# Kernel tuning notes

Measured on AMD Instinct MI355X. Metric: run time of the kernel, lower is better.

Reference implementation:

```python
import jax, jax.numpy as jnp
import numpy as np

VOCAB = 50000
WORD_DIM = 300
ENT_DIM = 128
ATT_DIM = 256
B, QLEN, DLEN = 64, 32, 2048
MUS = np.array([-0.9, -0.7, -0.5, -0.3, -0.1, 0.1, 0.3, 0.5, 0.7, 0.9, 1.0], dtype=np.float32)
SIGMAS = np.array([0.1] * 10 + [0.001], dtype=np.float32)


def setup_inputs() -> dict:
    key = jax.random.key(0)
    ks = jax.random.split(key, 12)
    # tokens in [-1, VOCAB-2]; -1 is padding (embed uses tok+1)
    query_tok = jax.random.randint(ks[0], (B, QLEN), -1, VOCAB - 1)
    doc_tok = jax.random.randint(ks[1], (B, DLEN), -1, VOCAB - 1)
    query_entity = jax.random.normal(ks[2], (B, QLEN, ENT_DIM), dtype=jnp.float32)
    doc_entity = jax.random.normal(ks[3], (B, DLEN, ENT_DIM), dtype=jnp.float32)
    embed_table = jax.random.normal(ks[4], (VOCAB, WORD_DIM), dtype=jnp.float32) * 0.1
    W_t = jax.random.normal(ks[5], (WORD_DIM, ATT_DIM), dtype=jnp.float32) * (1.0 / np.sqrt(WORD_DIM))
    b_t = jax.random.normal(ks[6], (ATT_DIM,), dtype=jnp.float32) * 0.01
    W_e = jax.random.normal(ks[7], (ENT_DIM, ATT_DIM), dtype=jnp.float32) * (1.0 / np.sqrt(ENT_DIM))
    b_e = jax.random.normal(ks[8], (ATT_DIM,), dtype=jnp.float32) * 0.01
    W_c = jax.random.normal(ks[9], (len(MUS), 1), dtype=jnp.float32) * 0.3
    b_c = jax.random.normal(ks[10], (1,), dtype=jnp.float32) * 0.01
    return {
        "query_tok": query_tok, "doc_tok": doc_tok,
        "query_entity": query_entity, "doc_entity": doc_entity,
        "embed_table": embed_table,
        "W_t": W_t, "b_t": b_t, "W_e": W_e, "b_e": b_e,
        "W_c": W_c, "b_c": b_c,
    }


def reference(query_tok, doc_tok, query_entity, doc_entity,
              embed_table, W_t, b_t, W_e, b_e, W_c, b_c):
    mus = jnp.asarray(MUS)
    sigmas = jnp.asarray(SIGMAS)
    # encode: embed(tok + 1)
    q_reps = embed_table[query_tok + 1]            # [B,Q,WORD]
    d_reps = embed_table[doc_tok + 1]              # [B,D,WORD]
    # transform_embed: relu(Linear(word) + Linear(entity))
    q = jax.nn.relu(q_reps @ W_t + b_t + query_entity @ W_e + b_e)  # [B,Q,A]
    d = jax.nn.relu(d_reps @ W_t + b_t + doc_entity @ W_e + b_e)    # [B,D,A]
    # SimmatModule: masked cosine similarity, VIEWS = 1
    qn = jnp.linalg.norm(q, axis=2)[:, :, None] + 1e-9              # [B,Q,1]
    dn = jnp.linalg.norm(d, axis=2)[:, None, :] + 1e-9              # [B,1,D]
    sim = jnp.einsum('bqa,bda->bqd', q, d) / (qn * dn)              # [B,Q,D]
    sim = jnp.where(query_tok[:, :, None] == -1, 0.0, sim)
    sim = jnp.where(doc_tok[:, None, :] == -1, 0.0, sim)
    # RBF kernel bank: exp(-0.5*(sim-mu)^2/sigma^2) -> [B,K,Q,D]
    adj = sim[:, None, :, :] - mus[None, :, None, None]
    kern = jnp.exp(-0.5 * adj * adj / (sigmas * sigmas)[None, :, None, None])
    result = kern.sum(axis=3)                                       # [B,K,Q]
    mask = (sim.sum(axis=2) != 0.0)[:, None, :]                     # [B,1,Q]
    mask = jnp.broadcast_to(mask, result.shape)
    result = jnp.where(mask, jnp.log(result + 1e-6), mask.astype(result.dtype))
    result = result.sum(axis=2)                                     # [B,K]
    scores = result @ W_c + b_c                                     # [B,1]
    return scores
```

## Files before the change

kernel.cpp:

```cpp
#include <hip/hip_runtime.h>
#include <math.h>

#define B_    64
#define QLEN  32
#define DLEN  2048
#define WORD  300
#define ENT   128
#define AD    256
#define NK    11
#define VOCAB 50000

typedef __bf16 bf16x8 __attribute__((ext_vector_type(8)));
typedef __bf16 bf16x4 __attribute__((ext_vector_type(4)));
typedef float  f32x4  __attribute__((ext_vector_type(4)));

__global__ __launch_bounds__(256) void knrm_wpack(
    const float* __restrict__ Wt, const float* __restrict__ We,
    const float* __restrict__ bt, const float* __restrict__ be,
    __bf16* __restrict__ Wtp, __bf16* __restrict__ Wep,
    float* __restrict__ bias)
{
    const int idx = blockIdx.x * 256 + threadIdx.x;
    if (idx < AD) bias[idx] = bt[idx] + be[idx];
    const int tile = idx >> 6, l = idx & 63;
    bf16x8 h;
    if (tile < 160) {
        const int s = tile >> 4, nb = tile & 15;
        const int col = nb * 16 + (l & 15);
        const int k0  = s * 32 + (l >> 4) * 8;
        #pragma unroll
        for (int j = 0; j < 8; ++j) {
            const int k = k0 + j;
            h[j] = (__bf16)((k < WORD) ? Wt[(size_t)k * AD + col] : 0.f);
        }
        *(bf16x8*)((char*)Wtp + (size_t)idx * 16) = h;
    } else {
        const int t2 = tile - 160;
        const int s = t2 >> 4, nb = t2 & 15;
        const int col = nb * 16 + (l & 15);
        const int k0  = s * 32 + (l >> 4) * 8;
        #pragma unroll
        for (int j = 0; j < 8; ++j)
            h[j] = (__bf16)We[(size_t)(k0 + j) * AD + col];
        *(bf16x8*)((char*)Wep + (size_t)(idx - 10240) * 16) = h;
    }
}

__global__ __launch_bounds__(256) void knrm_pgemm(
    const float* __restrict__ emb,
    const __bf16* __restrict__ Wtp,
    char* __restrict__ P)
{
    __shared__ __align__(16) char sm[40960];
    const int tid = threadIdx.x;
    const int v0  = blockIdx.x * 64;

    #pragma unroll
    for (int u = 0; u < 20; ++u) {
        const int idx  = u * 256 + tid;
        const int r    = idx / 80;
        const int slot = idx - r * 80;
        const int k    = slot * 4;
        f32x4 v = (f32x4){0.f, 0.f, 0.f, 0.f};
        if (k < WORD && v0 + r < VOCAB)
            v = *(const f32x4*)(emb + (size_t)(v0 + r) * WORD + k);
        bf16x4 hv;
        #pragma unroll
        for (int c = 0; c < 4; ++c) hv[c] = (__bf16)v[c];
        *(bf16x4*)(sm + ((r * 640 + slot * 8) ^ ((r & 7) << 4))) = hv;
    }
    __syncthreads();

    const int w  = tid >> 6;
    const int l  = tid & 63;
    const int lr = l & 15;
    const int lg = l >> 4;

    f32x4 acc[4][4];
    #pragma unroll
    for (int mf = 0; mf < 4; ++mf)
        #pragma unroll
        for (int nf = 0; nf < 4; ++nf)
            acc[mf][nf] = (f32x4){0.f, 0.f, 0.f, 0.f};

    #pragma unroll
    for (int t = 0; t < 10; ++t) {
        bf16x8 a[4];
        #pragma unroll
        for (int mf = 0; mf < 4; ++mf) {
            const int row = mf * 16 + lr;
            a[mf] = *(const bf16x8*)(sm +
                ((row * 640 + t * 64 + lg * 16) ^ ((row & 7) << 4)));
        }
        bf16x8 wv[4];
        #pragma unroll
        for (int nf = 0; nf < 4; ++nf) {
            const int tile = t * 16 + w * 4 + nf;
            wv[nf] = *(const bf16x8*)((const char*)Wtp + (size_t)tile * 1024 + l * 16);
        }
        #pragma unroll
        for (int mf = 0; mf < 4; ++mf)
            #pragma unroll
            for (int nf = 0; nf < 4; ++nf)
                acc[mf][nf] = __builtin_amdgcn_mfma_f32_16x16x32_bf16(
                    a[mf], wv[nf], acc[mf][nf], 0, 0, 0);
    }

    #pragma unroll
    for (int mf = 0; mf < 4; ++mf)
        #pragma unroll
        for (int reg = 0; reg < 4; ++reg) {
            const int v = v0 + mf * 16 + lg * 4 + reg;
            if (v < VOCAB) {
                bf16x4 h;
                #pragma unroll
                for (int nf = 0; nf < 4; ++nf) h[nf] = (__bf16)acc[mf][nf][reg];
                *(bf16x4*)(P + (size_t)v * 512 + w * 128 + lr * 8) = h;
            }
        }
}

__global__ __launch_bounds__(256) void knrm_qtrans(
    const int* __restrict__ tok,
    const float* __restrict__ ent,
    const char* __restrict__ Pp,
    const __bf16* __restrict__ Wep,
    const float* __restrict__ bias,
    char* __restrict__ qhatF)
{
    __shared__ __align__(16) char sm[16384 + 256];
    float* ssq  = (float*)(sm + 16384);
    int*   toks = (int*)(sm + 16384 + 128);

    const int tid  = threadIdx.x;
    const int row0 = blockIdx.x * 32;
    if (tid < 32) { toks[tid] = tok[row0 + tid] + 1; ssq[tid] = 0.f; }
    __syncthreads();

    const int wN = tid >> 6;
    const int l  = tid & 63;
    const int lr = l & 15;
    const int lg = l >> 4;
    const float* __restrict__ ebase = ent + (size_t)row0 * ENT;

    f32x4 acc[2][4];
    #pragma unroll
    for (int mf = 0; mf < 2; ++mf)
        #pragma unroll
        for (int nf = 0; nf < 4; ++nf)
            acc[mf][nf] = (f32x4){0.f, 0.f, 0.f, 0.f};

    bf16x4 pv[2][4];
    #pragma unroll
    for (int mf = 0; mf < 2; ++mf)
        #pragma unroll
        for (int reg = 0; reg < 4; ++reg) {
            const int r = mf * 16 + lg * 4 + reg;
            pv[mf][reg] = *(const bf16x4*)(Pp +
                (size_t)toks[r] * 512 + wN * 128 + lr * 8);
        }

    #pragma unroll
    for (int t = 0; t < 4; ++t) {
        bf16x8 a[2];
        #pragma unroll
        for (int mf = 0; mf < 2; ++mf) {
            const float* rp = ebase + (size_t)(mf * 16 + lr) * ENT + t * 32 + lg * 8;
            const f32x4 u0 = *(const f32x4*)rp;
            const f32x4 u1 = *(const f32x4*)(rp + 4);
            #pragma unroll
            for (int c = 0; c < 4; ++c) {
                a[mf][c]     = (__bf16)u0[c];
                a[mf][c + 4] = (__bf16)u1[c];
            }
        }
        bf16x8 wv[4];
        #pragma unroll
        for (int nf = 0; nf < 4; ++nf) {
            const int tile = t * 16 + wN * 4 + nf;
            wv[nf] = *(const bf16x8*)((const char*)Wep + (size_t)tile * 1024 + l * 16);
        }
        #pragma unroll
        for (int mf = 0; mf < 2; ++mf)
            #pragma unroll
            for (int nf = 0; nf < 4; ++nf)
                acc[mf][nf] = __builtin_amdgcn_mfma_f32_16x16x32_bf16(
                    a[mf], wv[nf], acc[mf][nf], 0, 0, 0);
    }

    float bv[4];
    #pragma unroll
    for (int nf = 0; nf < 4; ++nf) bv[nf] = bias[wN * 64 + nf * 16 + lr];
    float sq[2][4];
    #pragma unroll
    for (int mf = 0; mf < 2; ++mf)
        #pragma unroll
        for (int reg = 0; reg < 4; ++reg) {
            float s = 0.f;
            #pragma unroll
            for (int nf = 0; nf < 4; ++nf) {
                const float v = fmaxf(acc[mf][nf][reg] + (float)pv[mf][reg][nf]
                                      + bv[nf], 0.f);
                acc[mf][nf][reg] = v;
                s = fmaf(v, v, s);
            }
            sq[mf][reg] = s;
        }
    #pragma unroll
    for (int m = 1; m <= 8; m <<= 1)
        #pragma unroll
        for (int mf = 0; mf < 2; ++mf)
            #pragma unroll
            for (int reg = 0; reg < 4; ++reg)
                sq[mf][reg] += __shfl_xor(sq[mf][reg], m, 64);
    if (lr == 0) {
        #pragma unroll
        for (int mf = 0; mf < 2; ++mf)
            #pragma unroll
            for (int reg = 0; reg < 4; ++reg)
                atomicAdd(&ssq[mf * 16 + lg * 4 + reg], sq[mf][reg]);
    }
    #pragma unroll
    for (int mf = 0; mf < 2; ++mf)
        #pragma unroll
        for (int nf = 0; nf < 4; ++nf)
            #pragma unroll
            for (int reg = 0; reg < 4; ++reg) {
                const int r    = mf * 16 + lg * 4 + reg;
                const int col  = wN * 64 + nf * 16 + lr;
                const int byte = (r * 512 + col * 2) ^ ((r & 7) << 4);
                *(__bf16*)(sm + byte) = (__bf16)acc[mf][nf][reg];
            }
    __syncthreads();

    char* qb = qhatF + (size_t)blockIdx.x * 16384;
    #pragma unroll
    for (int it = 0; it < 4; ++it) {
        const int idx = it * 256 + tid;
        const int tile = idx >> 6, l2 = idx & 63;
        const int s  = tile >> 1, qt = tile & 1;
        const int row = qt * 16 + (l2 & 15);
        const int k0  = s * 32 + (l2 >> 4) * 8;
        const int byte = (row * 512 + k0 * 2) ^ ((row & 7) << 4);
        bf16x8 hv = *(const bf16x8*)(sm + byte);
        const float rn = (toks[row] == 0) ? 0.f
                                          : 1.f / (sqrtf(ssq[row]) + 1e-9f);
        #pragma unroll
        for (int j = 0; j < 8; ++j) hv[j] = (__bf16)((float)hv[j] * rn);
        *(bf16x8*)(qb + tile * 1024 + l2 * 16) = hv;
    }
}

__global__ __launch_bounds__(256) void knrm_fused2(
    const int* __restrict__ dtok,
    const float* __restrict__ dent,
    const char* __restrict__ Pp,
    const __bf16* __restrict__ Wep,
    const float* __restrict__ bias,
    const char* __restrict__ qhatF,
    float* __restrict__ ksum,
    float* __restrict__ simsum)
{
    __shared__ __align__(16) char sm[16384 + 256];
    float* ssq  = (float*)(sm + 16384);
    int*   toks = (int*)(sm + 16384 + 128);

    const int tid = threadIdx.x;
    const int b   = blockIdx.y;
    const int d0  = blockIdx.x * 32;
    const int drow0 = b * DLEN + d0;
    const int w  = tid >> 6;
    const int l  = tid & 63;
    const int lr = l & 15;
    const int lg = l >> 4;

    if (tid < 32) { toks[tid] = dtok[drow0 + tid] + 1; ssq[tid] = 0.f; }

    #pragma unroll
    for (int u = 0; u < 4; ++u) {
        const int slot = u * 256 + tid;
        const int r    = slot >> 5;
        const int c4   = (slot & 31) * 4;
        const f32x4 v = *(const f32x4*)(dent + (size_t)(drow0 + r) * ENT + c4);
        bf16x4 hv;
        #pragma unroll
        for (int c = 0; c < 4; ++c) hv[c] = (__bf16)v[c];
        *(bf16x4*)(sm + ((r * 256 + c4 * 2) ^ ((r & 7) << 4))) = hv;
    }
    __syncthreads();

    bf16x4 pv[2][4];
    #pragma unroll
    for (int mf = 0; mf < 2; ++mf)
        #pragma unroll
        for (int reg = 0; reg < 4; ++reg) {
            const int doc = mf * 16 + lg * 4 + reg;
            pv[mf][reg] = *(const bf16x4*)(Pp +
                (size_t)toks[doc] * 512 + w * 128 + lr * 8);
        }

    f32x4 acc[2][4];
    #pragma unroll
    for (int mf = 0; mf < 2; ++mf)
        #pragma unroll
        for (int nf = 0; nf < 4; ++nf)
            acc[mf][nf] = (f32x4){0.f, 0.f, 0.f, 0.f};

    #pragma unroll
    for (int t = 0; t < 4; ++t) {
        bf16x8 a[2];
        #pragma unroll
        for (int mf = 0; mf < 2; ++mf) {
            const int row = mf * 16 + lr;
            a[mf] = *(const bf16x8*)(sm +
                ((row * 256 + t * 64 + lg * 16) ^ ((row & 7) << 4)));
        }
        bf16x8 wv[4];
        #pragma unroll
        for (int nf = 0; nf < 4; ++nf) {
            const int tile = t * 16 + w * 4 + nf;
            wv[nf] = *(const bf16x8*)((const char*)Wep + (size_t)tile * 1024 + l * 16);
        }
        #pragma unroll
        for (int mf = 0; mf < 2; ++mf)
            #pragma unroll
            for (int nf = 0; nf < 4; ++nf)
                acc[mf][nf] = __builtin_amdgcn_mfma_f32_16x16x32_bf16(
                    a[mf], wv[nf], acc[mf][nf], 0, 0, 0);
    }
    __syncthreads();

    float bv[4];
    #pragma unroll
    for (int nf = 0; nf < 4; ++nf) bv[nf] = bias[w * 64 + nf * 16 + lr];
    float sq[2][4];
    #pragma unroll
    for (int mf = 0; mf < 2; ++mf)
        #pragma unroll
        for (int reg = 0; reg < 4; ++reg) {
            float s = 0.f;
            #pragma unroll
            for (int nf = 0; nf < 4; ++nf) {
                const float v = fmaxf(acc[mf][nf][reg] + (float)pv[mf][reg][nf]
                                      + bv[nf], 0.f);
                acc[mf][nf][reg] = v;
                s = fmaf(v, v, s);
            }
            sq[mf][reg] = s;
        }
    #pragma unroll
    for (int m = 1; m <= 8; m <<= 1)
        #pragma unroll
        for (int mf = 0; mf < 2; ++mf)
            #pragma unroll
            for (int reg = 0; reg < 4; ++reg)
                sq[mf][reg] += __shfl_xor(sq[mf][reg], m, 64);
    if (lr == 0) {
        #pragma unroll
        for (int mf = 0; mf < 2; ++mf)
            #pragma unroll
            for (int reg = 0; reg < 4; ++reg)
                atomicAdd(&ssq[mf * 16 + lg * 4 + reg], sq[mf][reg]);
    }
    #pragma unroll
    for (int mf = 0; mf < 2; ++mf)
        #pragma unroll
        for (int nf = 0; nf < 4; ++nf)
            #pragma unroll
            for (int reg = 0; reg < 4; ++reg) {
                const int doc  = mf * 16 + lg * 4 + reg;
                const int col  = w * 64 + nf * 16 + lr;
                const int byte = doc * 512 + ((col * 2) ^ ((doc & 15) << 4));
                *(__bf16*)(sm + byte) = (__bf16)acc[mf][nf][reg];
            }
    __syncthreads();

    const int dtile = w & 1, qtile = w >> 1;
    const int tdoc  = dtile * 16 + lr;
    const int q     = qtile * 16 + lr;
    const char* __restrict__ qb = qhatF + (size_t)b * 16384;
    f32x4 s0 = (f32x4){0.f, 0.f, 0.f, 0.f};
    #pragma unroll
    for (int s = 0; s < 8; ++s) {
        const bf16x8 ta = *(const bf16x8*)(sm +
            (tdoc * 512 + ((s * 64 + lg * 16) ^ ((tdoc & 15) << 4))));
        const bf16x8 qv = *(const bf16x8*)(qb + (s * 2 + qtile) * 1024 + l * 16);
        s0 = __builtin_amdgcn_mfma_f32_16x16x32_bf16(ta, qv, s0, 0, 0, 0);
    }

    float kq[12];
    #pragma unroll
    for (int k = 0; k < 12; ++k) kq[k] = 0.f;
    #pragma unroll
    for (int reg = 0; reg < 4; ++reg) {
        const int doc = dtile * 16 + lg * 4 + reg;
        const float dnv = (toks[doc] == 0) ? 0.f
                                           : 1.f / (sqrtf(ssq[doc]) + 1e-9f);
        const float sv = s0[reg] * dnv;
        kq[11] += sv;
        const float v5 = __expf(fmaf(10.f, sv, -50.f * sv * sv));
        const float gU = __expf(20.f * sv);
        const float gD = __expf(-20.f * sv);
        float u = v5;
        kq[5] += u * 0.60653066f;
        u *= gD; kq[4] += u * 0.60653066f;
        u *= gD; kq[3] += u * 0.011108997f;
        u *= gD; kq[2] += u * 3.7266532e-06f;
        u *= gD; kq[1] += u * 2.2895532e-11f;
        u *= gD; kq[0] += u * 2.5767571e-18f;
        u = v5;
        u *= gU; kq[6] += u * 0.011108997f;
        u *= gU; kq[7] += u * 3.7266532e-06f;
        u *= gU; kq[8] += u * 2.2895532e-11f;
        u *= gU; kq[9] += u * 2.5767571e-18f;
        const float t10 = sv - 1.0f;
        kq[10] += __expf(-500000.f * t10 * t10);
    }
    #pragma unroll
    for (int m = 16; m <= 32; m <<= 1)
        #pragma unroll
        for (int k = 0; k < 12; ++k)
            kq[k] += __shfl_xor(kq[k], m, 64);
    if (lg == 0) {
        #pragma unroll
        for (int k = 0; k < NK; ++k)
            atomicAdd(&ksum[((size_t)b * NK + k) * QLEN + q], kq[k]);
        atomicAdd(&simsum[b * QLEN + q], kq[11]);
    }
}

__global__ __launch_bounds__(384) void knrm_final(
    const float* __restrict__ ksum,
    const float* __restrict__ simsum,
    const float* __restrict__ Wc, const float* __restrict__ bc,
    float* __restrict__ out)
{
    __shared__ float redq[NK][QLEN];
    __shared__ float res[NK];
    const int b = blockIdx.x;
    const int t = threadIdx.x;
    if (t < NK * QLEN) {
        const int k = t >> 5;
        const int q = t & 31;
        const float ms = simsum[b * QLEN + q];
        redq[k][q] = (ms != 0.0f)
            ? logf(ksum[((size_t)b * NK + k) * QLEN + q] + 1e-6f)
            : 0.0f;
    }
    __syncthreads();
    if (t < NK) {
        float s = 0.f;
        for (int q = 0; q < QLEN; ++q) s += redq[t][q];
        res[t] = s;
    }
    __syncthreads();
    if (t == 0) {
        float s = bc[0];
        for (int k = 0; k < NK; ++k) s += res[k] * Wc[k];
        out[b] = s;
    }
}

extern "C" void kernel_launch(void* const* d_in, const int* in_sizes, int n_in,
                              void* d_out, int out_size, void* d_ws, size_t ws_size,
                              hipStream_t stream)
{
    (void)in_sizes; (void)n_in; (void)out_size; (void)ws_size;
    const int*   qtok = (const int*)d_in[0];
    const int*   dtok = (const int*)d_in[1];
    const float* qent = (const float*)d_in[2];
    const float* dent = (const float*)d_in[3];
    const float* emb  = (const float*)d_in[4];
    const float* Wt   = (const float*)d_in[5];
    const float* bt   = (const float*)d_in[6];
    const float* We   = (const float*)d_in[7];
    const float* be   = (const float*)d_in[8];
    const float* Wc   = (const float*)d_in[9];
    const float* bc   = (const float*)d_in[10];
    float* out = (float*)d_out;

    char* ws = (char*)d_ws;
    const size_t off_qhat = 0;
    const size_t off_Wtp  = off_qhat + 1048576;
    const size_t off_Wep  = off_Wtp  + 163840;
    const size_t off_bias = off_Wep  + 65536;
    const size_t off_ksum = off_bias + 1024;
    const size_t off_sim  = off_ksum + 90112;
    const size_t off_P    = off_sim  + 8192;

    char*   qhatF = ws + off_qhat;
    __bf16* Wtp   = (__bf16*)(ws + off_Wtp);
    __bf16* Wep   = (__bf16*)(ws + off_Wep);
    float*  bias  = (float*)(ws + off_bias);
    float*  ksum  = (float*)(ws + off_ksum);
    float*  simsum= (float*)(ws + off_sim);
    char*   P     = ws + off_P;

    hipMemsetAsync(ksum, 0, (size_t)(90112 + 8192), stream);

    knrm_wpack<<<dim3(56), dim3(256), 0, stream>>>(Wt, We, bt, be, Wtp, Wep, bias);
    knrm_pgemm<<<dim3((VOCAB + 63) / 64), dim3(256), 0, stream>>>(emb, Wtp, P);
    knrm_qtrans<<<dim3(64), dim3(256), 0, stream>>>(
        qtok, qent, P, Wep, bias, qhatF);
    knrm_fused2<<<dim3(DLEN / 32, B_), dim3(256), 0, stream>>>(
        dtok, dent, P, Wep, bias, qhatF, ksum, simsum);
    knrm_final<<<dim3(B_), dim3(384), 0, stream>>>(ksum, simsum, Wc, bc, out);
}
```

Baseline: 90.52 us.

## Process four doc tiles per block with register-prefetched double-buffered entity loads

The fused doc kernel now loops over four 32-doc tiles per block instead of one. While the current tile is computed, it prefetches the next tile's entity rows and projected-embedding rows into registers, then writes them into an alternate shared-memory buffer. The goal is to hide global-load latency and amortise per-block setup such as bias loads and launch overhead. In exchange the grid shrinks fourfold, to 1024 blocks, shared memory roughly doubles, and register pressure rises, all of which can hurt occupancy.

```diff
diff --git a/kernel.cpp b/kernel.cpp
--- a/kernel.cpp
+++ b/kernel.cpp
@@ -9,6 +9,7 @@
 #define AD    256
 #define NK    11
 #define VOCAB 50000
+#define TPB   4
 
 typedef __bf16 bf16x8 __attribute__((ext_vector_type(8)));
 typedef __bf16 bf16x4 __attribute__((ext_vector_type(4)));
@@ -251,7 +252,7 @@
     }
 }
 
-__global__ __launch_bounds__(256) void knrm_fused2(
+__global__ __launch_bounds__(256) void knrm_fused3(
     const int* __restrict__ dtok,
     const float* __restrict__ dent,
     const char* __restrict__ Pp,
@@ -261,20 +262,21 @@
     float* __restrict__ ksum,
     float* __restrict__ simsum)
 {
-    __shared__ __align__(16) char sm[16384 + 256];
-    float* ssq  = (float*)(sm + 16384);
-    int*   toks = (int*)(sm + 16384 + 128);
+    __shared__ __align__(16) char sm[33536];
+    float* ssqb = (float*)(sm + 32768);
+    int*   toks = (int*)(sm + 33024);
 
     const int tid = threadIdx.x;
     const int b   = blockIdx.y;
-    const int d0  = blockIdx.x * 32;
+    const int d0  = blockIdx.x * (TPB * 32);
     const int drow0 = b * DLEN + d0;
     const int w  = tid >> 6;
     const int l  = tid & 63;
     const int lr = l & 15;
     const int lg = l >> 4;
 
-    if (tid < 32) { toks[tid] = dtok[drow0 + tid] + 1; ssq[tid] = 0.f; }
+    if (tid < TPB * 32) toks[tid] = dtok[drow0 + tid] + 1;
+    if (tid < 64) ssqb[tid] = 0.f;
 
     #pragma unroll
     for (int u = 0; u < 4; ++u) {
@@ -299,133 +301,185 @@
                 (size_t)toks[doc] * 512 + w * 128 + lr * 8);
         }
 
-    f32x4 acc[2][4];
-    #pragma unroll
-    for (int mf = 0; mf < 2; ++mf)
-        #pragma unroll
-        for (int nf = 0; nf < 4; ++nf)
-            acc[mf][nf] = (f32x4){0.f, 0.f, 0.f, 0.f};
-
-    #pragma unroll
-    for (int t = 0; t < 4; ++t) {
-        bf16x8 a[2];
-        #pragma unroll
-        for (int mf = 0; mf < 2; ++mf) {
-            const int row = mf * 16 + lr;
-            a[mf] = *(const bf16x8*)(sm +
-                ((row * 256 + t * 64 + lg * 16) ^ ((row & 7) << 4)));
-        }
-        bf16x8 wv[4];
-        #pragma unroll
-        for (int nf = 0; nf < 4; ++nf) {
-            const int tile = t * 16 + w * 4 + nf;
-            wv[nf] = *(const bf16x8*)((const char*)Wep + (size_t)tile * 1024 + l * 16);
-        }
+    float bv[4];
+    #pragma unroll
+    for (int nf = 0; nf < 4; ++nf) bv[nf] = bias[w * 64 + nf * 16 + lr];
+
+    const char* __restrict__ qb = qhatF + (size_t)b * 16384;
+    const int dtile = w & 1, qtile = w >> 1;
+    const int q = qtile * 16 + lr;
+
+    #pragma unroll
+    for (int t = 0; t < TPB; ++t) {
+        const int cur = t & 1;
+        float* ssq = ssqb + cur * 32;
+
+        f32x4 dnx[4];
+        bf16x4 pvN[2][4];
+        if (t + 1 < TPB) {
+            #pragma unroll
+            for (int u = 0; u < 4; ++u) {
+                const int slot = u * 256 + tid;
+                const int r    = slot >> 5;
+                const int c4   = (slot & 31) * 4;
+                dnx[u] = *(const f32x4*)(dent +
+                    (size_t)(drow0 + (t + 1) * 32 + r) * ENT + c4);
+            }
+            #pragma unroll
+            for (int mf = 0; mf < 2; ++mf)
+                #pragma unroll
+                for (int reg = 0; reg < 4; ++reg) {
+                    const int doc = (t + 1) * 32 + mf * 16 + lg * 4 + reg;
+                    pvN[mf][reg] = *(const bf16x4*)(Pp +
+                        (size_t)toks[doc] * 512 + w * 128 + lr * 8);
+                }
+        }
+
+        f32x4 acc[2][4];
         #pragma unroll
         for (int mf = 0; mf < 2; ++mf)
             #pragma unroll
             for (int nf = 0; nf < 4; ++nf)
-                acc[mf][nf] = __builtin_amdgcn_mfma_f32_16x16x32_bf16(
-                    a[mf], wv[nf], acc[mf][nf], 0, 0, 0);
-    }
-    __syncthreads();
-
-    float bv[4];
-    #pragma unroll
-    for (int nf = 0; nf < 4; ++nf) bv[nf] = bias[w * 64 + nf * 16 + lr];
-    float sq[2][4];
-    #pragma unroll
-    for (int mf = 0; mf < 2; ++mf)
+                acc[mf][nf] = (f32x4){0.f, 0.f, 0.f, 0.f};
+
+        #pragma unroll
+        for (int tk = 0; tk < 4; ++tk) {
+            bf16x8 a[2];
+            #pragma unroll
+            for (int mf = 0; mf < 2; ++mf) {
+                const int row = mf * 16 + lr;
+                a[mf] = *(const bf16x8*)(sm + cur * 8192 +
+                    ((row * 256 + tk * 64 + lg * 16) ^ ((row & 7) << 4)));
+            }
+            bf16x8 wv[4];
+            #pragma unroll
+            for (int nf = 0; nf < 4; ++nf) {
+                const int tile = tk * 16 + w * 4 + nf;
+                wv[nf] = *(const bf16x8*)((const char*)Wep +
+                                          (size_t)tile * 1024 + l * 16);
+            }
+            #pragma unroll
+            for (int mf = 0; mf < 2; ++mf)
+                #pragma unroll
+                for (int nf = 0; nf < 4; ++nf)
+                    acc[mf][nf] = __builtin_amdgcn_mfma_f32_16x16x32_bf16(
+                        a[mf], wv[nf], acc[mf][nf], 0, 0, 0);
+        }
+
+        if (tid < 32) ssqb[(cur ^ 1) * 32 + tid] = 0.f;
+
+        float sq[2][4];
+        #pragma unroll
+        for (int mf = 0; mf < 2; ++mf)
+            #pragma unroll
+            for (int reg = 0; reg < 4; ++reg) {
+                float s = 0.f;
+                #pragma unroll
+                for (int nf = 0; nf < 4; ++nf) {
+                    const float v = fmaxf(acc[mf][nf][reg] +
+                                          (float)pv[mf][reg][nf] + bv[nf], 0.f);
+                    acc[mf][nf][reg] = v;
+                    s = fmaf(v, v, s);
+                }
+                sq[mf][reg] = s;
+            }
+        #pragma unroll
+        for (int m = 1; m <= 8; m <<= 1)
+            #pragma unroll
+            for (int mf = 0; mf < 2; ++mf)
+                #pragma unroll
+                for (int reg = 0; reg < 4; ++reg)
+                    sq[mf][reg] += __shfl_xor(sq[mf][reg], m, 64);
+        if (lr == 0) {
+            #pragma unroll
+            for (int mf = 0; mf < 2; ++mf)
+                #pragma unroll
+                for (int reg = 0; reg < 4; ++reg)
+                    atomicAdd(&ssq[mf * 16 + lg * 4 + reg], sq[mf][reg]);
+        }
+        #pragma unroll
+        for (int mf = 0; mf < 2; ++mf)
+            #pragma unroll
+            for (int nf = 0; nf < 4; ++nf)
+                #pragma unroll
+                for (int reg = 0; reg < 4; ++reg) {
+                    const int doc  = mf * 16 + lg * 4 + reg;
+                    const int col  = w * 64 + nf * 16 + lr;
+                    const int byte = 16384 + doc * 512 +
+                                     ((col * 2) ^ ((doc & 15) << 4));
+                    *(__bf16*)(sm + byte) = (__bf16)acc[mf][nf][reg];
+                }
+        __syncthreads();
+
+        const int tdoc = dtile * 16 + lr;
+        f32x4 s0 = (f32x4){0.f, 0.f, 0.f, 0.f};
+        #pragma unroll
+        for (int s = 0; s < 8; ++s) {
+            const bf16x8 ta = *(const bf16x8*)(sm + 16384 + tdoc * 512 +
+                ((s * 64 + lg * 16) ^ ((tdoc & 15) << 4)));
+            const bf16x8 qv = *(const bf16x8*)(qb + (s * 2 + qtile) * 1024 + l * 16);
+            s0 = __builtin_amdgcn_mfma_f32_16x16x32_bf16(ta, qv, s0, 0, 0, 0);
+        }
+
+        float kq[12];
+        #pragma unroll
+        for (int k = 0; k < 12; ++k) kq[k] = 0.f;
         #pragma unroll
         for (int reg = 0; reg < 4; ++reg) {
-            float s = 0.f;
-            #pragma unroll
-            for (int nf = 0; nf < 4; ++nf) {
-                const float v = fmaxf(acc[mf][nf][reg] + (float)pv[mf][reg][nf]
-                                      + bv[nf], 0.f);
-                acc[mf][nf][reg] = v;
-                s = fmaf(v, v, s);
-            }
-            sq[mf][reg] = s;
-        }
-    #pragma unroll
-    for (int m = 1; m <= 8; m <<= 1)
-        #pragma unroll
-        for (int mf = 0; mf < 2; ++mf)
-            #pragma unroll
-            for (int reg = 0; reg < 4; ++reg)
-                sq[mf][reg] += __shfl_xor(sq[mf][reg], m, 64);
-    if (lr == 0) {
-        #pragma unroll
-        for (int mf = 0; mf < 2; ++mf)
-            #pragma unroll
-            for (int reg = 0; reg < 4; ++reg)
-                atomicAdd(&ssq[mf * 16 + lg * 4 + reg], sq[mf][reg]);
-    }
-    #pragma unroll
-    for (int mf = 0; mf < 2; ++mf)
-        #pragma unroll
-        for (int nf = 0; nf < 4; ++nf)
-            #pragma unroll
-            for (int reg = 0; reg < 4; ++reg) {
-                const int doc  = mf * 16 + lg * 4 + reg;
-                const int col  = w * 64 + nf * 16 + lr;
-                const int byte = doc * 512 + ((col * 2) ^ ((doc & 15) << 4));
-                *(__bf16*)(sm + byte) = (__bf16)acc[mf][nf][reg];
-            }
-    __syncthreads();
-
-    const int dtile = w & 1, qtile = w >> 1;
-    const int tdoc  = dtile * 16 + lr;
-    const int q     = qtile * 16 + lr;
-    const char* __restrict__ qb = qhatF + (size_t)b * 16384;
-    f32x4 s0 = (f32x4){0.f, 0.f, 0.f, 0.f};
-    #pragma unroll
-    for (int s = 0; s < 8; ++s) {
-        const bf16x8 ta = *(const bf16x8*)(sm +
-            (tdoc * 512 + ((s * 64 + lg * 16) ^ ((tdoc & 15) << 4))));
-        const bf16x8 qv = *(const bf16x8*)(qb + (s * 2 + qtile) * 1024 + l * 16);
-        s0 = __builtin_amdgcn_mfma_f32_16x16x32_bf16(ta, qv, s0, 0, 0, 0);
-    }
-
-    float kq[12];
-    #pragma unroll
-    for (int k = 0; k < 12; ++k) kq[k] = 0.f;
-    #pragma unroll
-    for (int reg = 0; reg < 4; ++reg) {
-        const int doc = dtile * 16 + lg * 4 + reg;
-        const float dnv = (toks[doc] == 0) ? 0.f
-                                           : 1.f / (sqrtf(ssq[doc]) + 1e-9f);
-        const float sv = s0[reg] * dnv;
-        kq[11] += sv;
-        const float v5 = __expf(fmaf(10.f, sv, -50.f * sv * sv));
-        const float gU = __expf(20.f * sv);
-        const float gD = __expf(-20.f * sv);
-        float u = v5;
-        kq[5] += u * 0.60653066f;
-        u *= gD; kq[4] += u * 0.60653066f;
-        u *= gD; kq[3] += u * 0.011108997f;
-        u *= gD; kq[2] += u * 3.7266532e-06f;
-        u *= gD; kq[1] += u * 2.2895532e-11f;
-        u *= gD; kq[0] += u * 2.5767571e-18f;
-        u = v5;
-        u *= gU; kq[6] += u * 0.011108997f;
-        u *= gU; kq[7] += u * 3.7266532e-06f;
-        u *= gU; kq[8] += u * 2.2895532e-11f;
-        u *= gU; kq[9] += u * 2.5767571e-18f;
-        const float t10 = sv - 1.0f;
-        kq[10] += __expf(-500000.f * t10 * t10);
-    }
-    #pragma unroll
-    for (int m = 16; m <= 32; m <<= 1)
-        #pragma unroll
-        for (int k = 0; k < 12; ++k)
-            kq[k] += __shfl_xor(kq[k], m, 64);
-    if (lg == 0) {
-        #pragma unroll
-        for (int k = 0; k < NK; ++k)
-            atomicAdd(&ksum[((size_t)b * NK + k) * QLEN + q], kq[k]);
-        atomicAdd(&simsum[b * QLEN + q], kq[11]);
+            const int doc = dtile * 16 + lg * 4 + reg;
+            const float dnv = (toks[t * 32 + doc] == 0) ? 0.f
+                              : 1.f / (sqrtf(ssq[doc]) + 1e-9f);
+            const float sv = s0[reg] * dnv;
+            kq[11] += sv;
+            const float v5 = __expf(fmaf(10.f, sv, -50.f * sv * sv));
+            const float gU = __expf(20.f * sv);
+            const float gD = __expf(-20.f * sv);
+            float u = v5;
+            kq[5] += u * 0.60653066f;
+            u *= gD; kq[4] += u * 0.60653066f;
+            u *= gD; kq[3] += u * 0.011108997f;
+            u *= gD; kq[2] += u * 3.7266532e-06f;
+            u *= gD; kq[1] += u * 2.2895532e-11f;
+            u *= gD; kq[0] += u * 2.5767571e-18f;
+            u = v5;
+            u *= gU; kq[6] += u * 0.011108997f;
+            u *= gU; kq[7] += u * 3.7266532e-06f;
+            u *= gU; kq[8] += u * 2.2895532e-11f;
+            u *= gU; kq[9] += u * 2.5767571e-18f;
+            const float t10 = sv - 1.0f;
+            kq[10] += __expf(-500000.f * t10 * t10);
+        }
+        #pragma unroll
+        for (int m = 16; m <= 32; m <<= 1)
+            #pragma unroll
+            for (int k = 0; k < 12; ++k)
+                kq[k] += __shfl_xor(kq[k], m, 64);
+        if (lg == 0) {
+            #pragma unroll
+            for (int k = 0; k < NK; ++k)
+                atomicAdd(&ksum[((size_t)b * NK + k) * QLEN + q], kq[k]);
+            atomicAdd(&simsum[b * QLEN + q], kq[11]);
+        }
+
+        if (t + 1 < TPB) {
+            #pragma unroll
+            for (int u = 0; u < 4; ++u) {
+                const int slot = u * 256 + tid;
+                const int r    = slot >> 5;
+                const int c4   = (slot & 31) * 4;
+                bf16x4 hv;
+                #pragma unroll
+                for (int c = 0; c < 4; ++c) hv[c] = (__bf16)dnx[u][c];
+                *(bf16x4*)(sm + (cur ^ 1) * 8192 +
+                           ((r * 256 + c4 * 2) ^ ((r & 7) << 4))) = hv;
+            }
+            #pragma unroll
+            for (int mf = 0; mf < 2; ++mf)
+                #pragma unroll
+                for (int reg = 0; reg < 4; ++reg)
+                    pv[mf][reg] = pvN[mf][reg];
+            __syncthreads();
+        }
     }
 }
 
@@ -502,7 +556,7 @@
     knrm_pgemm<<<dim3((VOCAB + 63) / 64), dim3(256), 0, stream>>>(emb, Wtp, P);
     knrm_qtrans<<<dim3(64), dim3(256), 0, stream>>>(
         qtok, qent, P, Wep, bias, qhatF);
-    knrm_fused2<<<dim3(DLEN / 32, B_), dim3(256), 0, stream>>>(
+    knrm_fused3<<<dim3(DLEN / (TPB * 32), B_), dim3(256), 0, stream>>>(
         dtok, dent, P, Wep, bias, qhatF, ksum, simsum);
     knrm_final<<<dim3(B_), dim3(384), 0, stream>>>(ksum, simsum, Wc, bc, out);
 }
```

New measurement: 93.22 us. 3.0% more time.

## Make each wave own 16 doc rows end-to-end, removing block barriers

Applied to the files above, without the earlier changes.

The doc kernel is restructured so each wave computes all 256 attention columns for its own 16 documents. It then normalizes them in registers, writes them to a private LDS tile and runs the similarity MFMA against both query tiles. This removes the cross-wave LDS atomics for norms and the block-wide __syncthreads, and loads doc entities straight from global memory. The P table layout is permuted so each lane fetches its 16 columns with two 16-byte loads. The cost is more accumulator registers (16 f32x4 plus kq[2][12]), which may lower occupancy, and twice the LDS per block.

```diff
diff --git a/kernel.cpp b/kernel.cpp
--- a/kernel.cpp
+++ b/kernel.cpp
@@ -115,7 +115,7 @@
                 bf16x4 h;
                 #pragma unroll
                 for (int nf = 0; nf < 4; ++nf) h[nf] = (__bf16)acc[mf][nf][reg];
-                *(bf16x4*)(P + (size_t)v * 512 + w * 128 + lr * 8) = h;
+                *(bf16x4*)(P + (size_t)v * 512 + lr * 32 + w * 8) = h;
             }
         }
 }
@@ -157,7 +157,7 @@
         for (int reg = 0; reg < 4; ++reg) {
             const int r = mf * 16 + lg * 4 + reg;
             pv[mf][reg] = *(const bf16x4*)(Pp +
-                (size_t)toks[r] * 512 + wN * 128 + lr * 8);
+                (size_t)toks[r] * 512 + lr * 32 + wN * 8);
         }
 
     #pragma unroll
@@ -251,7 +251,7 @@
     }
 }
 
-__global__ __launch_bounds__(256) void knrm_fused2(
+__global__ __launch_bounds__(256) void knrm_fused4(
     const int* __restrict__ dtok,
     const float* __restrict__ dent,
     const char* __restrict__ Pp,
@@ -261,171 +261,148 @@
     float* __restrict__ ksum,
     float* __restrict__ simsum)
 {
-    __shared__ __align__(16) char sm[16384 + 256];
-    float* ssq  = (float*)(sm + 16384);
-    int*   toks = (int*)(sm + 16384 + 128);
-
+    __shared__ __align__(16) char sm[32768];
     const int tid = threadIdx.x;
     const int b   = blockIdx.y;
-    const int d0  = blockIdx.x * 32;
-    const int drow0 = b * DLEN + d0;
-    const int w  = tid >> 6;
-    const int l  = tid & 63;
-    const int lr = l & 15;
-    const int lg = l >> 4;
-
-    if (tid < 32) { toks[tid] = dtok[drow0 + tid] + 1; ssq[tid] = 0.f; }
-
-    #pragma unroll
-    for (int u = 0; u < 4; ++u) {
-        const int slot = u * 256 + tid;
-        const int r    = slot >> 5;
-        const int c4   = (slot & 31) * 4;
-        const f32x4 v = *(const f32x4*)(dent + (size_t)(drow0 + r) * ENT + c4);
-        bf16x4 hv;
-        #pragma unroll
-        for (int c = 0; c < 4; ++c) hv[c] = (__bf16)v[c];
-        *(bf16x4*)(sm + ((r * 256 + c4 * 2) ^ ((r & 7) << 4))) = hv;
-    }
-    __syncthreads();
-
-    bf16x4 pv[2][4];
-    #pragma unroll
-    for (int mf = 0; mf < 2; ++mf)
-        #pragma unroll
-        for (int reg = 0; reg < 4; ++reg) {
-            const int doc = mf * 16 + lg * 4 + reg;
-            pv[mf][reg] = *(const bf16x4*)(Pp +
-                (size_t)toks[doc] * 512 + w * 128 + lr * 8);
-        }
-
-    f32x4 acc[2][4];
-    #pragma unroll
-    for (int mf = 0; mf < 2; ++mf)
-        #pragma unroll
-        for (int nf = 0; nf < 4; ++nf)
-            acc[mf][nf] = (f32x4){0.f, 0.f, 0.f, 0.f};
-
+    const int w   = tid >> 6;
+    const int l   = tid & 63;
+    const int lr  = l & 15;
+    const int lg  = l >> 4;
+    const int dW    = blockIdx.x * 64 + w * 16;
+    const int drowW = b * DLEN + dW;
+    char* T = sm + w * 8192;
+
+    int tk[4];
+    #pragma unroll
+    for (int reg = 0; reg < 4; ++reg)
+        tk[reg] = dtok[drowW + lg * 4 + reg] + 1;
+
+    bf16x8 pvl[4], pvh[4];
+    #pragma unroll
+    for (int reg = 0; reg < 4; ++reg) {
+        const char* p = Pp + (size_t)tk[reg] * 512 + lr * 32;
+        pvl[reg] = *(const bf16x8*)p;
+        pvh[reg] = *(const bf16x8*)(p + 16);
+    }
+
+    f32x4 acc[16];
+    #pragma unroll
+    for (int nf = 0; nf < 16; ++nf) acc[nf] = (f32x4){0.f, 0.f, 0.f, 0.f};
+
+    const float* __restrict__ drow = dent + (size_t)(drowW + lr) * ENT;
     #pragma unroll
     for (int t = 0; t < 4; ++t) {
-        bf16x8 a[2];
-        #pragma unroll
-        for (int mf = 0; mf < 2; ++mf) {
-            const int row = mf * 16 + lr;
-            a[mf] = *(const bf16x8*)(sm +
-                ((row * 256 + t * 64 + lg * 16) ^ ((row & 7) << 4)));
-        }
-        bf16x8 wv[4];
-        #pragma unroll
-        for (int nf = 0; nf < 4; ++nf) {
-            const int tile = t * 16 + w * 4 + nf;
-            wv[nf] = *(const bf16x8*)((const char*)Wep + (size_t)tile * 1024 + l * 16);
-        }
-        #pragma unroll
-        for (int mf = 0; mf < 2; ++mf)
-            #pragma unroll
-            for (int nf = 0; nf < 4; ++nf)
-                acc[mf][nf] = __builtin_amdgcn_mfma_f32_16x16x32_bf16(
-                    a[mf], wv[nf], acc[mf][nf], 0, 0, 0);
-    }
-    __syncthreads();
-
-    float bv[4];
-    #pragma unroll
-    for (int nf = 0; nf < 4; ++nf) bv[nf] = bias[w * 64 + nf * 16 + lr];
-    float sq[2][4];
-    #pragma unroll
-    for (int mf = 0; mf < 2; ++mf)
-        #pragma unroll
-        for (int reg = 0; reg < 4; ++reg) {
-            float s = 0.f;
-            #pragma unroll
-            for (int nf = 0; nf < 4; ++nf) {
-                const float v = fmaxf(acc[mf][nf][reg] + (float)pv[mf][reg][nf]
-                                      + bv[nf], 0.f);
-                acc[mf][nf][reg] = v;
-                s = fmaf(v, v, s);
-            }
-            sq[mf][reg] = s;
-        }
+        const float* rp = drow + t * 32 + lg * 8;
+        const f32x4 u0 = *(const f32x4*)rp;
+        const f32x4 u1 = *(const f32x4*)(rp + 4);
+        bf16x8 a;
+        #pragma unroll
+        for (int c = 0; c < 4; ++c) {
+            a[c]     = (__bf16)u0[c];
+            a[c + 4] = (__bf16)u1[c];
+        }
+        #pragma unroll
+        for (int nf = 0; nf < 16; ++nf) {
+            const bf16x8 wv = *(const bf16x8*)((const char*)Wep +
+                (size_t)(t * 16 + nf) * 1024 + l * 16);
+            acc[nf] = __builtin_amdgcn_mfma_f32_16x16x32_bf16(a, wv, acc[nf], 0, 0, 0);
+        }
+    }
+
+    float ssq[4] = {0.f, 0.f, 0.f, 0.f};
+    #pragma unroll
+    for (int nf = 0; nf < 16; ++nf) {
+        const float bvn = bias[nf * 16 + lr];
+        #pragma unroll
+        for (int reg = 0; reg < 4; ++reg) {
+            const float pvv = (nf < 8) ? (float)pvl[reg][nf]
+                                       : (float)pvh[reg][nf - 8];
+            const float v = fmaxf(acc[nf][reg] + pvv + bvn, 0.f);
+            acc[nf][reg] = v;
+            ssq[reg] = fmaf(v, v, ssq[reg]);
+        }
+    }
     #pragma unroll
     for (int m = 1; m <= 8; m <<= 1)
         #pragma unroll
-        for (int mf = 0; mf < 2; ++mf)
-            #pragma unroll
-            for (int reg = 0; reg < 4; ++reg)
-                sq[mf][reg] += __shfl_xor(sq[mf][reg], m, 64);
-    if (lr == 0) {
-        #pragma unroll
-        for (int mf = 0; mf < 2; ++mf)
-            #pragma unroll
-            for (int reg = 0; reg < 4; ++reg)
-                atomicAdd(&ssq[mf * 16 + lg * 4 + reg], sq[mf][reg]);
-    }
-    #pragma unroll
-    for (int mf = 0; mf < 2; ++mf)
-        #pragma unroll
-        for (int nf = 0; nf < 4; ++nf)
-            #pragma unroll
-            for (int reg = 0; reg < 4; ++reg) {
-                const int doc  = mf * 16 + lg * 4 + reg;
-                const int col  = w * 64 + nf * 16 + lr;
-                const int byte = doc * 512 + ((col * 2) ^ ((doc & 15) << 4));
-                *(__bf16*)(sm + byte) = (__bf16)acc[mf][nf][reg];
-            }
-    __syncthreads();
-
-    const int dtile = w & 1, qtile = w >> 1;
-    const int tdoc  = dtile * 16 + lr;
-    const int q     = qtile * 16 + lr;
+        for (int reg = 0; reg < 4; ++reg)
+            ssq[reg] += __shfl_xor(ssq[reg], m, 64);
+    float dnv[4];
+    #pragma unroll
+    for (int reg = 0; reg < 4; ++reg)
+        dnv[reg] = (tk[reg] == 0) ? 0.f : 1.f / (sqrtf(ssq[reg]) + 1e-9f);
+
+    #pragma unroll
+    for (int nf = 0; nf < 16; ++nf)
+        #pragma unroll
+        for (int reg = 0; reg < 4; ++reg) {
+            const int d    = lg * 4 + reg;
+            const int byte = d * 512 + (((nf * 16 + lr) * 2) ^ (d << 4));
+            *(__bf16*)(T + byte) = (__bf16)(acc[nf][reg] * dnv[reg]);
+        }
+    asm volatile("s_waitcnt lgkmcnt(0)" ::: "memory");
+    __builtin_amdgcn_sched_barrier(0);
+
     const char* __restrict__ qb = qhatF + (size_t)b * 16384;
-    f32x4 s0 = (f32x4){0.f, 0.f, 0.f, 0.f};
+    f32x4 sacc[2];
+    sacc[0] = (f32x4){0.f, 0.f, 0.f, 0.f};
+    sacc[1] = (f32x4){0.f, 0.f, 0.f, 0.f};
     #pragma unroll
     for (int s = 0; s < 8; ++s) {
-        const bf16x8 ta = *(const bf16x8*)(sm +
-            (tdoc * 512 + ((s * 64 + lg * 16) ^ ((tdoc & 15) << 4))));
-        const bf16x8 qv = *(const bf16x8*)(qb + (s * 2 + qtile) * 1024 + l * 16);
-        s0 = __builtin_amdgcn_mfma_f32_16x16x32_bf16(ta, qv, s0, 0, 0, 0);
-    }
-
-    float kq[12];
-    #pragma unroll
-    for (int k = 0; k < 12; ++k) kq[k] = 0.f;
-    #pragma unroll
-    for (int reg = 0; reg < 4; ++reg) {
-        const int doc = dtile * 16 + lg * 4 + reg;
-        const float dnv = (toks[doc] == 0) ? 0.f
-                                           : 1.f / (sqrtf(ssq[doc]) + 1e-9f);
-        const float sv = s0[reg] * dnv;
-        kq[11] += sv;
-        const float v5 = __expf(fmaf(10.f, sv, -50.f * sv * sv));
-        const float gU = __expf(20.f * sv);
-        const float gD = __expf(-20.f * sv);
-        float u = v5;
-        kq[5] += u * 0.60653066f;
-        u *= gD; kq[4] += u * 0.60653066f;
-        u *= gD; kq[3] += u * 0.011108997f;
-        u *= gD; kq[2] += u * 3.7266532e-06f;
-        u *= gD; kq[1] += u * 2.2895532e-11f;
-        u *= gD; kq[0] += u * 2.5767571e-18f;
-        u = v5;
-        u *= gU; kq[6] += u * 0.011108997f;
-        u *= gU; kq[7] += u * 3.7266532e-06f;
-        u *= gU; kq[8] += u * 2.2895532e-11f;
-        u *= gU; kq[9] += u * 2.5767571e-18f;
-        const float t10 = sv - 1.0f;
-        kq[10] += __expf(-500000.f * t10 * t10);
-    }
+        const bf16x8 ta = *(const bf16x8*)(T + lr * 512 +
+            ((s * 64 + lg * 16) ^ (lr << 4)));
+        #pragma unroll
+        for (int qt = 0; qt < 2; ++qt) {
+            const bf16x8 qv = *(const bf16x8*)(qb + (s * 2 + qt) * 1024 + l * 16);
+            sacc[qt] = __builtin_amdgcn_mfma_f32_16x16x32_bf16(ta, qv, sacc[qt], 0, 0, 0);
+        }
+    }
+
+    float kq[2][12];
+    #pragma unroll
+    for (int qt = 0; qt < 2; ++qt)
+        #pragma unroll
+        for (int k = 0; k < 12; ++k) kq[qt][k] = 0.f;
+    #pragma unroll
+    for (int qt = 0; qt < 2; ++qt)
+        #pragma unroll
+        for (int reg = 0; reg < 4; ++reg) {
+            const float sv = sacc[qt][reg];
+            kq[qt][11] += sv;
+            const float v5 = __expf(fmaf(10.f, sv, -50.f * sv * sv));
+            const float gU = __expf(20.f * sv);
+            const float gD = __expf(-20.f * sv);
+            float u = v5;
+            kq[qt][5] += u * 0.60653066f;
+            u *= gD; kq[qt][4] += u * 0.60653066f;
+            u *= gD; kq[qt][3] += u * 0.011108997f;
+            u *= gD; kq[qt][2] += u * 3.7266532e-06f;
+            u *= gD; kq[qt][1] += u * 2.2895532e-11f;
+            u *= gD; kq[qt][0] += u * 2.5767571e-18f;
+            u = v5;
+            u *= gU; kq[qt][6] += u * 0.011108997f;
+            u *= gU; kq[qt][7] += u * 3.7266532e-06f;
+            u *= gU; kq[qt][8] += u * 2.2895532e-11f;
+            u *= gU; kq[qt][9] += u * 2.5767571e-18f;
+            const float t10 = sv - 1.0f;
+            kq[qt][10] += __expf(-500000.f * t10 * t10);
+        }
     #pragma unroll
     for (int m = 16; m <= 32; m <<= 1)
         #pragma unroll
-        for (int k = 0; k < 12; ++k)
-            kq[k] += __shfl_xor(kq[k], m, 64);
+        for (int qt = 0; qt < 2; ++qt)
+            #pragma unroll
+            for (int k = 0; k < 12; ++k)
+                kq[qt][k] += __shfl_xor(kq[qt][k], m, 64);
     if (lg == 0) {
         #pragma unroll
-        for (int k = 0; k < NK; ++k)
-            atomicAdd(&ksum[((size_t)b * NK + k) * QLEN + q], kq[k]);
-        atomicAdd(&simsum[b * QLEN + q], kq[11]);
+        for (int qt = 0; qt < 2; ++qt) {
+            const int q = qt * 16 + lr;
+            #pragma unroll
+            for (int k = 0; k < NK; ++k)
+                atomicAdd(&ksum[((size_t)b * NK + k) * QLEN + q], kq[qt][k]);
+            atomicAdd(&simsum[b * QLEN + q], kq[qt][11]);
+        }
     }
 }
 
@@ -502,7 +479,7 @@
     knrm_pgemm<<<dim3((VOCAB + 63) / 64), dim3(256), 0, stream>>>(emb, Wtp, P);
     knrm_qtrans<<<dim3(64), dim3(256), 0, stream>>>(
         qtok, qent, P, Wep, bias, qhatF);
-    knrm_fused2<<<dim3(DLEN / 32, B_), dim3(256), 0, stream>>>(
+    knrm_fused4<<<dim3(DLEN / 64, B_), dim3(256), 0, stream>>>(
         dtok, dent, P, Wep, bias, qhatF, ksum, simsum);
     knrm_final<<<dim3(B_), dim3(384), 0, stream>>>(ksum, simsum, Wc, bc, out);
 }
```

After: 106.9 us. 1.18x slower.

## Split fused doc kernel into similarity GEMM and separate RBF reduction kernel

Applied to the files above, without the earlier changes.

Splits the fused document kernel in two. The first kernel computes the doc projection and the cosine similarity matrix and writes it to a workspace buffer in fp32. A second kernel reads that matrix and evaluates the RBF kernel bank with a block-level shared-memory reduction before the global atomics. This is meant to lower register pressure and atomic contention in the fused kernel, at the cost of an extra 16 MB round trip through global memory and one more launch; it falls back to the old kernel if the workspace is too small.

```diff
diff --git a/kernel.cpp b/kernel.cpp
--- a/kernel.cpp
+++ b/kernel.cpp
@@ -248,6 +248,151 @@
         #pragma unroll
         for (int j = 0; j < 8; ++j) hv[j] = (__bf16)((float)hv[j] * rn);
         *(bf16x8*)(qb + tile * 1024 + l2 * 16) = hv;
+    }
+}
+
+__global__ __launch_bounds__(256) void knrm_fused5(
+    const int* __restrict__ dtok,
+    const float* __restrict__ dent,
+    const char* __restrict__ Pp,
+    const __bf16* __restrict__ Wep,
+    const float* __restrict__ bias,
+    const char* __restrict__ qhatF,
+    float* __restrict__ simsO)
+{
+    __shared__ __align__(16) char sm[16384 + 256];
+    float* ssq  = (float*)(sm + 16384);
+    int*   toks = (int*)(sm + 16384 + 128);
+
+    const int tid = threadIdx.x;
+    const int b   = blockIdx.y;
+    const int d0  = blockIdx.x * 32;
+    const int drow0 = b * DLEN + d0;
+    const int w  = tid >> 6;
+    const int l  = tid & 63;
+    const int lr = l & 15;
+    const int lg = l >> 4;
+
+    if (tid < 32) { toks[tid] = dtok[drow0 + tid] + 1; ssq[tid] = 0.f; }
+
+    #pragma unroll
+    for (int u = 0; u < 4; ++u) {
+        const int slot = u * 256 + tid;
+        const int r    = slot >> 5;
+        const int c4   = (slot & 31) * 4;
+        const f32x4 v = *(const f32x4*)(dent + (size_t)(drow0 + r) * ENT + c4);
+        bf16x4 hv;
+        #pragma unroll
+        for (int c = 0; c < 4; ++c) hv[c] = (__bf16)v[c];
+        *(bf16x4*)(sm + ((r * 256 + c4 * 2) ^ ((r & 7) << 4))) = hv;
+    }
+    __syncthreads();
+
+    bf16x4 pv[2][4];
+    #pragma unroll
+    for (int mf = 0; mf < 2; ++mf)
+        #pragma unroll
+        for (int reg = 0; reg < 4; ++reg) {
+            const int doc = mf * 16 + lg * 4 + reg;
+            pv[mf][reg] = *(const bf16x4*)(Pp +
+                (size_t)toks[doc] * 512 + w * 128 + lr * 8);
+        }
+
+    f32x4 acc[2][4];
+    #pragma unroll
+    for (int mf = 0; mf < 2; ++mf)
+        #pragma unroll
+        for (int nf = 0; nf < 4; ++nf)
+            acc[mf][nf] = (f32x4){0.f, 0.f, 0.f, 0.f};
+
+    #pragma unroll
+    for (int t = 0; t < 4; ++t) {
+        bf16x8 a[2];
+        #pragma unroll
+        for (int mf = 0; mf < 2; ++mf) {
+            const int row = mf * 16 + lr;
+            a[mf] = *(const bf16x8*)(sm +
+                ((row * 256 + t * 64 + lg * 16) ^ ((row & 7) << 4)));
+        }
+        bf16x8 wv[4];
+        #pragma unroll
+        for (int nf = 0; nf < 4; ++nf) {
+            const int tile = t * 16 + w * 4 + nf;
+            wv[nf] = *(const bf16x8*)((const char*)Wep + (size_t)tile * 1024 + l * 16);
+        }
+        #pragma unroll
+        for (int mf = 0; mf < 2; ++mf)
+            #pragma unroll
+            for (int nf = 0; nf < 4; ++nf)
+                acc[mf][nf] = __builtin_amdgcn_mfma_f32_16x16x32_bf16(
+                    a[mf], wv[nf], acc[mf][nf], 0, 0, 0);
+    }
+    __syncthreads();
+
+    float bv[4];
+    #pragma unroll
+    for (int nf = 0; nf < 4; ++nf) bv[nf] = bias[w * 64 + nf * 16 + lr];
+    float sq[2][4];
+    #pragma unroll
+    for (int mf = 0; mf < 2; ++mf)
+        #pragma unroll
+        for (int reg = 0; reg < 4; ++reg) {
+            float s = 0.f;
+            #pragma unroll
+            for (int nf = 0; nf < 4; ++nf) {
+                const float v = fmaxf(acc[mf][nf][reg] + (float)pv[mf][reg][nf]
+                                      + bv[nf], 0.f);
+                acc[mf][nf][reg] = v;
+                s = fmaf(v, v, s);
+            }
+            sq[mf][reg] = s;
+        }
+    #pragma unroll
+    for (int m = 1; m <= 8; m <<= 1)
+        #pragma unroll
+        for (int mf = 0; mf < 2; ++mf)
+            #pragma unroll
+            for (int reg = 0; reg < 4; ++reg)
+                sq[mf][reg] += __shfl_xor(sq[mf][reg], m, 64);
+    if (lr == 0) {
+        #pragma unroll
+        for (int mf = 0; mf < 2; ++mf)
+            #pragma unroll
+            for (int reg = 0; reg < 4; ++reg)
+                atomicAdd(&ssq[mf * 16 + lg * 4 + reg], sq[mf][reg]);
+    }
+    #pragma unroll
+    for (int mf = 0; mf < 2; ++mf)
+        #pragma unroll
+        for (int nf = 0; nf < 4; ++nf)
+            #pragma unroll
+            for (int reg = 0; reg < 4; ++reg) {
+                const int doc  = mf * 16 + lg * 4 + reg;
+                const int col  = w * 64 + nf * 16 + lr;
+                const int byte = doc * 512 + ((col * 2) ^ ((doc & 15) << 4));
+                *(__bf16*)(sm + byte) = (__bf16)acc[mf][nf][reg];
+            }
+    __syncthreads();
+
+    const int dtile = w & 1, qtile = w >> 1;
+    const int tdoc  = dtile * 16 + lr;
+    const char* __restrict__ qb = qhatF + (size_t)b * 16384;
+    f32x4 s0 = (f32x4){0.f, 0.f, 0.f, 0.f};
+    #pragma unroll
+    for (int s = 0; s < 8; ++s) {
+        const bf16x8 ta = *(const bf16x8*)(sm +
+            (tdoc * 512 + ((s * 64 + lg * 16) ^ ((tdoc & 15) << 4))));
+        const bf16x8 qv = *(const bf16x8*)(qb + (s * 2 + qtile) * 1024 + l * 16);
+        s0 = __builtin_amdgcn_mfma_f32_16x16x32_bf16(ta, qv, s0, 0, 0, 0);
+    }
+
+    float* so = simsO + ((size_t)b * DLEN + d0) * QLEN;
+    #pragma unroll
+    for (int reg = 0; reg < 4; ++reg) {
+        const int doc = dtile * 16 + lg * 4 + reg;
+        const float dnv = (toks[doc] == 0) ? 0.f
+                                           : 1.f / (sqrtf(ssq[doc]) + 1e-9f);
+        so[(size_t)doc * QLEN + qtile * 16 + lr] = s0[reg] * dnv;
     }
 }
 
@@ -429,6 +574,64 @@
     }
 }
 
+__global__ __launch_bounds__(256) void knrm_rbf(
+    const float* __restrict__ simsI,
+    float* __restrict__ ksum,
+    float* __restrict__ simsum)
+{
+    __shared__ float red[384];
+    const int tid = threadIdx.x;
+    const int b   = blockIdx.y;
+    const int d0  = blockIdx.x * 128;
+    const int q   = tid & 31;
+    for (int i = tid; i < 384; i += 256) red[i] = 0.f;
+    __syncthreads();
+
+    const float* __restrict__ base = simsI + ((size_t)b * DLEN + d0) * QLEN;
+    float kq[12];
+    #pragma unroll
+    for (int k = 0; k < 12; ++k) kq[k] = 0.f;
+
+    #pragma unroll
+    for (int u = 0; u < 16; ++u) {
+        const float sv = base[u * 256 + tid];
+        kq[11] += sv;
+        const float v5 = __expf(fmaf(10.f, sv, -50.f * sv * sv));
+        const float gU = __expf(20.f * sv);
+        const float gD = __expf(-20.f * sv);
+        float t = v5;
+        kq[5] += t * 0.60653066f;
+        t *= gD; kq[4] += t * 0.60653066f;
+        t *= gD; kq[3] += t * 0.011108997f;
+        t *= gD; kq[2] += t * 3.7266532e-06f;
+        t *= gD; kq[1] += t * 2.2895532e-11f;
+        t *= gD; kq[0] += t * 2.5767571e-18f;
+        t = v5;
+        t *= gU; kq[6] += t * 0.011108997f;
+        t *= gU; kq[7] += t * 3.7266532e-06f;
+        t *= gU; kq[8] += t * 2.2895532e-11f;
+        t *= gU; kq[9] += t * 2.5767571e-18f;
+        const float t10 = sv - 1.0f;
+        kq[10] += __expf(-500000.f * t10 * t10);
+    }
+
+    #pragma unroll
+    for (int k = 0; k < 12; ++k)
+        kq[k] += __shfl_xor(kq[k], 32, 64);
+    if ((tid & 63) < 32) {
+        #pragma unroll
+        for (int k = 0; k < 12; ++k)
+            atomicAdd(&red[k * 32 + q], kq[k]);
+    }
+    __syncthreads();
+
+    for (int i = tid; i < 384; i += 256) {
+        const int k = i >> 5, qq = i & 31;
+        if (k < NK) atomicAdd(&ksum[((size_t)b * NK + k) * QLEN + qq], red[i]);
+        else        atomicAdd(&simsum[b * QLEN + qq], red[i]);
+    }
+}
+
 __global__ __launch_bounds__(384) void knrm_final(
     const float* __restrict__ ksum,
     const float* __restrict__ simsum,
@@ -465,7 +668,7 @@
                               void* d_out, int out_size, void* d_ws, size_t ws_size,
                               hipStream_t stream)
 {
-    (void)in_sizes; (void)n_in; (void)out_size; (void)ws_size;
+    (void)in_sizes; (void)n_in; (void)out_size;
     const int*   qtok = (const int*)d_in[0];
     const int*   dtok = (const int*)d_in[1];
     const float* qent = (const float*)d_in[2];
@@ -487,6 +690,7 @@
     const size_t off_ksum = off_bias + 1024;
     const size_t off_sim  = off_ksum + 90112;
     const size_t off_P    = off_sim  + 8192;
+    const size_t off_sims = off_P    + 25600000;
 
     char*   qhatF = ws + off_qhat;
     __bf16* Wtp   = (__bf16*)(ws + off_Wtp);
@@ -495,6 +699,9 @@
     float*  ksum  = (float*)(ws + off_ksum);
     float*  simsum= (float*)(ws + off_sim);
     char*   P     = ws + off_P;
+    float*  simsX = (float*)(ws + off_sims);
+
+    const bool big = ws_size >= off_sims + (size_t)B_ * DLEN * QLEN * 4;
 
     hipMemsetAsync(ksum, 0, (size_t)(90112 + 8192), stream);
 
@@ -502,7 +709,13 @@
     knrm_pgemm<<<dim3((VOCAB + 63) / 64), dim3(256), 0, stream>>>(emb, Wtp, P);
     knrm_qtrans<<<dim3(64), dim3(256), 0, stream>>>(
         qtok, qent, P, Wep, bias, qhatF);
-    knrm_fused2<<<dim3(DLEN / 32, B_), dim3(256), 0, stream>>>(
-        dtok, dent, P, Wep, bias, qhatF, ksum, simsum);
+    if (big) {
+        knrm_fused5<<<dim3(DLEN / 32, B_), dim3(256), 0, stream>>>(
+            dtok, dent, P, Wep, bias, qhatF, simsX);
+        knrm_rbf<<<dim3(16, B_), dim3(256), 0, stream>>>(simsX, ksum, simsum);
+    } else {
+        knrm_fused2<<<dim3(DLEN / 32, B_), dim3(256), 0, stream>>>(
+            dtok, dent, P, Wep, bias, qhatF, ksum, simsum);
+    }
     knrm_final<<<dim3(B_), dim3(384), 0, stream>>>(ksum, simsum, Wc, bc, out);
 }
```

Measured after the change: 86.98 us. 3.9% less time.
